# Performance work log

Hardware: AMD Instinct MI355X
Metric: run time of the kernel (lower is better)

The kernel has to match this reference:

```python
import jax, jax.numpy as jnp
import numpy as np

L = 4        # num_layers
D = 64       # in_channels == hidden_channels
OUT = 1      # out_channels
N = 50000    # nodes
E = 800000   # edges
G = 64       # graphs in batch
EPS = 1e-5


def setup_inputs() -> dict:
    key = jax.random.key(0)
    ks = jax.random.split(key, 16)
    s = 1.0 / np.sqrt(D)
    inp = {
        "x": jax.random.normal(ks[0], (N, D), jnp.float32),
        "edge_index": jax.random.randint(ks[1], (2, E), 0, N, jnp.int32),
        "batch": jnp.sort(jax.random.randint(ks[2], (N,), 0, G, jnp.int32)),
        # per-layer GNLayer params (stacked over L)
        "Wm1": jax.random.uniform(ks[3], (L, D, D), jnp.float32, -s, s),
        "bm1": jnp.zeros((L, D), jnp.float32),
        "Wm2": jax.random.uniform(ks[4], (L, D, D), jnp.float32, -s, s),
        "bm2": jnp.zeros((L, D), jnp.float32),
        "Wr": jax.random.uniform(ks[5], (L, D, D), jnp.float32, -s, s),
        "br": jnp.zeros((L, D), jnp.float32),
        "a_conv": jnp.full((L,), 0.25, jnp.float32),     # PReLU slopes
        "gamma": jnp.ones((L, D), jnp.float32),
        "beta": jnp.zeros((L, D), jnp.float32),
        # MLP head
        "Wh1": jax.random.uniform(ks[6], (D, D), jnp.float32, -s, s),
        "bh1": jnp.zeros((D,), jnp.float32),
        "Wh2": jax.random.uniform(ks[7], (D, OUT), jnp.float32, -s, s),
        "bh2": jnp.zeros((OUT,), jnp.float32),
        "a_head": jnp.float32(0.25),
    }
    return inp


def _prelu(v, a):
    return jnp.where(v >= 0, v, a * v)


def reference(x, edge_index, batch, Wm1, bm1, Wm2, bm2, Wr, br, a_conv,
              gamma, beta, Wh1, bh1, Wh2, bh2, a_head):
    src, dst = edge_index[0], edge_index[1]
    h = x
    for i in range(L):
        # GNLayer: message MLP on source features, sum-aggregate at dst, + root transform
        m = jax.nn.relu(h[src] @ Wm1[i] + bm1[i]) @ Wm2[i] + bm2[i]   # [E, D]
        agg = jax.ops.segment_sum(m, dst, num_segments=N)              # [N, D]
        h = agg + h @ Wr[i] + br[i]
        # PReLU
        h = _prelu(h, a_conv[i])
        # BatchNorm over the node dimension (training-mode batch stats)
        mu = jnp.mean(h, axis=0)
        var = jnp.var(h, axis=0)
        h = gamma[i] * (h - mu) * jax.lax.rsqrt(var + EPS) + beta[i]
    # global_mean_pool over graphs
    sums = jax.ops.segment_sum(h, batch, num_segments=G)               # [G, D]
    cnts = jax.ops.segment_sum(jnp.ones((N, 1), h.dtype), batch, num_segments=G)
    g = sums / jnp.maximum(cnts, 1.0)
    # MLP head
    out = _prelu(g @ Wh1 + bh1, a_head) @ Wh2 + bh2                    # [G, OUT]
    return out
```

## Files before the change

kernel.cpp:

```cpp
#include <hip/hip_runtime.h>
#include <hip/hip_fp16.h>

#define D 64


__global__ __launch_bounds__(256) void hist_kernel(const int* __restrict__ dst,
                                                   int* __restrict__ cnt, int E) {
  int e = blockIdx.x * 256 + threadIdx.x;
  if (e < E) atomicAdd(&cnt[dst[e]], 1);
}

__global__ __launch_bounds__(1024) void scan_partial_kernel(const int* __restrict__ cnt,
                                                            int* __restrict__ bsum, int N) {
  __shared__ int lds[1024];
  int i = blockIdx.x * 1024 + threadIdx.x;
  lds[threadIdx.x] = (i < N) ? cnt[i] : 0;
  __syncthreads();
  for (int off = 512; off > 0; off >>= 1) {
    if (threadIdx.x < off) lds[threadIdx.x] += lds[threadIdx.x + off];
    __syncthreads();
  }
  if (threadIdx.x == 0) bsum[blockIdx.x] = lds[0];
}

__global__ void scan_bsum_kernel(int* __restrict__ bsum, int nb,
                                 int* __restrict__ row_ptr, int N, int E) {
  int tid = threadIdx.x;
  int o = (tid < nb) ? bsum[tid] : 0;
  int v = o;
  for (int off = 1; off < 64; off <<= 1) {
    int t = __shfl_up(v, off, 64);
    if (tid >= off) v += t;
  }
  if (tid < nb) bsum[tid] = v - o;
  if (tid == 0) row_ptr[N] = E;
}

__global__ __launch_bounds__(1024) void scan_final_kernel(const int* __restrict__ cnt,
                                                          const int* __restrict__ bsum,
                                                          int* __restrict__ row_ptr,
                                                          int* __restrict__ cursor, int N) {
  __shared__ int lds[1024];
  int tid = threadIdx.x;
  int i = blockIdx.x * 1024 + tid;
  int v = (i < N) ? cnt[i] : 0;
  lds[tid] = v;
  __syncthreads();
  for (int off = 1; off < 1024; off <<= 1) {
    int t = (tid >= off) ? lds[tid - off] : 0;
    __syncthreads();
    lds[tid] += t;
    __syncthreads();
  }
  if (i < N) {
    int excl = bsum[blockIdx.x] + lds[tid] - v;
    row_ptr[i] = excl;
    cursor[i] = excl;
  }
}

__global__ __launch_bounds__(256) void scatter_kernel(const int* __restrict__ srcs,
                                                      const int* __restrict__ dst,
                                                      int* __restrict__ cursor,
                                                      int* __restrict__ csr_src, int E) {
  int e = blockIdx.x * 256 + threadIdx.x;
  if (e < E) {
    int p = atomicAdd(&cursor[dst[e]], 1);
    csr_src[p] = srcs[e];
  }
}


__global__ __launch_bounds__(256, 4) void node_mlp_kernel(
    const float* __restrict__ hin, const float* __restrict__ bnS, const float* __restrict__ bnSS,
    const float* __restrict__ gammaL, const float* __restrict__ betaL,
    const float* __restrict__ W1, const float* __restrict__ b1,
    const float* __restrict__ W2, const float* __restrict__ b2,
    __half* __restrict__ Rout, float* __restrict__ HRout, int N) {
  __shared__ float2 w12[D * D];
  __shared__ float hrow[32][D];
  const int tid = threadIdx.x;
  for (int i = tid; i < D * D; i += 256) w12[i] = make_float2(W1[i], W2[i]);
  const int c = tid & 63;
  const int w = tid >> 6;
  float sc = 1.f, sh = 0.f;
  if (bnS) {
    float invN = 1.f / (float)N;
    float mu = bnS[c] * invN;
    float var = bnSS[c] * invN - mu * mu;
    float s = gammaL[c] * rsqrtf(var + 1e-5f);
    sc = s;
    sh = betaL[c] - mu * s;
  }
  const float bb1 = b1[c], bb2 = b2[c];
  const int ntiles = (N + 31) >> 5;
  for (int t = blockIdx.x; t < ntiles; t += gridDim.x) {
    const int base = t * 32;
    __syncthreads();
#pragma unroll
    for (int j = 0; j < 8; ++j) {
      int r = 4 * j + w;
      int row = base + r;
      float v = (row < N) ? hin[(size_t)row * D + c] : 0.f;
      hrow[r][c] = v * sc + sh;
    }
    __syncthreads();
    float a1[8], a2[8];
#pragma unroll
    for (int j = 0; j < 8; ++j) { a1[j] = bb1; a2[j] = bb2; }
    for (int k = 0; k < D; k += 4) {
      const float2 wa = w12[(k + 0) * D + c];
      const float2 wb = w12[(k + 1) * D + c];
      const float2 wc = w12[(k + 2) * D + c];
      const float2 wd = w12[(k + 3) * D + c];
#pragma unroll
      for (int j = 0; j < 8; ++j) {
        const float4 h4 = *(const float4*)&hrow[w * 8 + j][k];
        a1[j] += h4.x * wa.x + h4.y * wb.x + h4.z * wc.x + h4.w * wd.x;
        a2[j] += h4.x * wa.y + h4.y * wb.y + h4.z * wc.y + h4.w * wd.y;
      }
    }
#pragma unroll
    for (int j = 0; j < 8; ++j) {
      int row = base + w * 8 + j;
      if (row < N) {
        Rout[(size_t)row * D + c] = __float2half(fmaxf(a1[j], 0.f));
        HRout[(size_t)row * D + c] = a2[j];
      }
    }
  }
}


__device__ __forceinline__ float lane_bcast(float v, int lane) {
  return __int_as_float(__builtin_amdgcn_readlane(__float_as_int(v), lane));
}
__device__ __forceinline__ int lane_bcast_i(int v, int lane) {
  return __builtin_amdgcn_readlane(v, lane);
}

__global__ __launch_bounds__(256) void agg_kernel(const int* __restrict__ row_ptr,
                                                  const int* __restrict__ csr_src,
                                                  const __half* __restrict__ Rm,
                                                  const float* __restrict__ HRm,
                                                  const float* __restrict__ W2m,
                                                  const float* __restrict__ b2m,
                                                  const float* __restrict__ aconv,
                                                  float* __restrict__ hout,
                                                  float* __restrict__ bnsum,
                                                  float* __restrict__ bnsumsq, int N) {
  __shared__ float w2[D * D];
  __shared__ float red[4][D];
  __shared__ float red2[4][D];
  const int tid = threadIdx.x;
  const int c = tid & 63;
  const int w = tid >> 6;
  const int q = c & 15;
  const int eg = c >> 4;
  for (int i = tid; i < D * D; i += 256) w2[i] = W2m[i];
  const float alpha = *aconv;
  const float bb = b2m[c];
  const int NW = gridDim.x * 4;
  float psum = 0.f, psumsq = 0.f;
  __syncthreads();

  int n = blockIdx.x * 4 + w;
  int e0 = 0, e1 = 0, idx = 0;
  if (n < N) {
    e0 = row_ptr[n];
    e1 = row_ptr[n + 1];
    int m = e1 - e0;
    if (m > 64) m = 64;
    if (m > 0) idx = csr_src[e0 + (c < m ? c : m - 1)];
  }
  while (n < N) {
    const int n2 = n + NW;
    int e0n = 0, e1n = 0, idxn = 0;
    if (n2 < N) {
      e0n = row_ptr[n2];
      e1n = row_ptr[n2 + 1];
      int mn = e1n - e0n;
      if (mn > 64) mn = 64;
      if (mn > 0) idxn = csr_src[e0n + (c < mn ? c : mn - 1)];
    }
    const int deg = e1 - e0;
    float acc0 = 0.f, acc1 = 0.f, acc2 = 0.f, acc3 = 0.f;
    int kb = 0;
    int curidx = idx;
    while (kb < deg) {
      int m = deg - kb;
      if (m > 64) m = 64;
      if (kb > 0) curidx = csr_src[e0 + kb + (c < m ? c : m - 1)];
      int j = 0;
      for (; j + 3 < m; j += 4) {
        const int s = __shfl(curidx, j + eg, 64);
        const uint2 rv = *(const uint2*)(Rm + (size_t)s * D + (q << 2));
        const float2 f01 = __half22float2(*(const __half2*)&rv.x);
        const float2 f23 = __half22float2(*(const __half2*)&rv.y);
        acc0 += f01.x;
        acc1 += f01.y;
        acc2 += f23.x;
        acc3 += f23.y;
      }
      for (; j < m; ++j) {
        const int s = lane_bcast_i(curidx, j);
        if (eg == 0) {
          const uint2 rv = *(const uint2*)(Rm + (size_t)s * D + (q << 2));
          const float2 f01 = __half22float2(*(const __half2*)&rv.x);
          const float2 f23 = __half22float2(*(const __half2*)&rv.y);
          acc0 += f01.x;
          acc1 += f01.y;
          acc2 += f23.x;
          acc3 += f23.y;
        }
      }
      kb += m;
    }
    acc0 += __shfl_xor(acc0, 16, 64);
    acc1 += __shfl_xor(acc1, 16, 64);
    acc2 += __shfl_xor(acc2, 16, 64);
    acc3 += __shfl_xor(acc3, 16, 64);
    acc0 += __shfl_xor(acc0, 32, 64);
    acc1 += __shfl_xor(acc1, 32, 64);
    acc2 += __shfl_xor(acc2, 32, 64);
    acc3 += __shfl_xor(acc3, 32, 64);
    const float degf = (float)deg;
    float o0 = bb * degf + HRm[(size_t)n * D + c];
    float o1 = 0.f, o2 = 0.f, o3 = 0.f;
#pragma unroll
    for (int kk = 0; kk < D; kk += 4) {
      const int src = kk >> 2;
      o0 += lane_bcast(acc0, src) * w2[(kk + 0) * D + c];
      o1 += lane_bcast(acc1, src) * w2[(kk + 1) * D + c];
      o2 += lane_bcast(acc2, src) * w2[(kk + 2) * D + c];
      o3 += lane_bcast(acc3, src) * w2[(kk + 3) * D + c];
    }
    const float o = (o0 + o1) + (o2 + o3);
    const float h2 = (o >= 0.f) ? o : alpha * o;
    hout[(size_t)n * D + c] = h2;
    psum += h2;
    psumsq += h2 * h2;
    n = n2;
    e0 = e0n;
    e1 = e1n;
    idx = idxn;
  }
  red[w][c] = psum;
  red2[w][c] = psumsq;
  __syncthreads();
  if (w == 0) {
    float s = red[0][c] + red[1][c] + red[2][c] + red[3][c];
    float ss = red2[0][c] + red2[1][c] + red2[2][c] + red2[3][c];
    atomicAdd(&bnsum[c], s);
    atomicAdd(&bnsumsq[c], ss);
  }
}


__global__ __launch_bounds__(256) void pool_head_kernel(
    const float* __restrict__ h, const float* __restrict__ bnS, const float* __restrict__ bnSS,
    const float* __restrict__ gammaL, const float* __restrict__ betaL,
    const int* __restrict__ batch, const float* __restrict__ Wh1, const float* __restrict__ bh1,
    const float* __restrict__ Wh2, const float* __restrict__ bh2,
    const float* __restrict__ ahead, float* __restrict__ out, int N) {
  const int g = blockIdx.x;
  const int tid = threadIdx.x;
  const int c = tid & 63;
  const int w = tid >> 6;
  float sc, sh;
  {
    float invN = 1.f / (float)N;
    float mu = bnS[c] * invN;
    float var = bnSS[c] * invN - mu * mu;
    float s = gammaL[c] * rsqrtf(var + 1e-5f);
    sc = s;
    sh = betaL[c] - mu * s;
  }
  int s0, s1;
  {
    int lo = 0, hi = N;
    while (lo < hi) { int mid = (lo + hi) >> 1; if (batch[mid] < g) lo = mid + 1; else hi = mid; }
    s0 = lo;
    lo = s0; hi = N;
    while (lo < hi) { int mid = (lo + hi) >> 1; if (batch[mid] < g + 1) lo = mid + 1; else hi = mid; }
    s1 = lo;
  }
  float sum = 0.f;
  for (int r = s0 + w; r < s1; r += 4) sum += h[(size_t)r * D + c] * sc + sh;
  __shared__ float red[4][D];
  __shared__ float mean[D];
  red[w][c] = sum;
  __syncthreads();
  if (tid < D) {
    float cnt = (float)(s1 - s0);
    mean[c] = (red[0][c] + red[1][c] + red[2][c] + red[3][c]) / fmaxf(cnt, 1.0f);
  }
  __syncthreads();
  if (tid < D) {
    int j = tid;
    float a = bh1[j];
#pragma unroll
    for (int k = 0; k < D; ++k) a += mean[k] * Wh1[k * D + j];
    float al = *ahead;
    float v = (a >= 0.f) ? a : al * a;
    float pval = v * Wh2[j];
    for (int off = 32; off > 0; off >>= 1) pval += __shfl_down(pval, off, 64);
    if (j == 0) out[g] = pval + bh2[0];
  }
}


extern "C" void kernel_launch(void* const* d_in, const int* in_sizes, int n_in,
                              void* d_out, int out_size, void* d_ws, size_t ws_size,
                              hipStream_t stream) {
  const float* x = (const float*)d_in[0];
  const int* ei = (const int*)d_in[1];
  const int* batch = (const int*)d_in[2];
  const float* Wm1 = (const float*)d_in[3];
  const float* bm1 = (const float*)d_in[4];
  const float* Wm2 = (const float*)d_in[5];
  const float* bm2 = (const float*)d_in[6];
  const float* Wr = (const float*)d_in[7];
  const float* br = (const float*)d_in[8];
  const float* aconv = (const float*)d_in[9];
  const float* gamma = (const float*)d_in[10];
  const float* beta = (const float*)d_in[11];
  const float* Wh1 = (const float*)d_in[12];
  const float* bh1 = (const float*)d_in[13];
  const float* Wh2 = (const float*)d_in[14];
  const float* bh2 = (const float*)d_in[15];
  const float* ahead = (const float*)d_in[16];

  const int N = in_sizes[0] / D;
  const int E = in_sizes[1] / 2;
  const int L = in_sizes[3] / (D * D);
  const int G = out_size;

  const int* srcs = ei;
  const int* dsts = ei + E;

  char* p = (char*)d_ws;
  auto alloc = [&](size_t bytes) {
    char* r = p;
    p += (bytes + 255) & ~(size_t)255;
    return r;
  };
  int* row_ptr = (int*)alloc((size_t)(N + 1) * 4);
  int* cursor = (int*)alloc((size_t)N * 4);
  int* bsum = (int*)alloc(64 * 4);
  int* csr_src = (int*)alloc((size_t)E * 4);
  __half* Rbuf = (__half*)alloc((size_t)N * D * 2);
  float* HRbuf = (float*)alloc((size_t)N * D * 4);
  float* hbuf = (float*)alloc((size_t)N * D * 4);
  float* bnsum = (float*)alloc((size_t)L * D * 4 * 2);
  float* bnsumsq = bnsum + (size_t)L * D;

  hipMemsetAsync(row_ptr, 0, (size_t)((char*)(cursor + N) - (char*)row_ptr), stream);
  hipMemsetAsync(bnsum, 0, (size_t)L * D * 4 * 2, stream);

  const int nb = (N + 1023) / 1024;
  hist_kernel<<<(E + 255) / 256, 256, 0, stream>>>(dsts, cursor, E);
  scan_partial_kernel<<<nb, 1024, 0, stream>>>(cursor, bsum, N);
  scan_bsum_kernel<<<1, 64, 0, stream>>>(bsum, nb, row_ptr, N, E);
  scan_final_kernel<<<nb, 1024, 0, stream>>>(cursor, bsum, row_ptr, cursor, N);
  scatter_kernel<<<(E + 255) / 256, 256, 0, stream>>>(srcs, dsts, cursor, csr_src, E);

  const int ntiles = (N + 31) / 32;

  const float* hin = x;
  const float* bnS = nullptr;
  const float* bnSS = nullptr;
  const float* gmL = nullptr;
  const float* btL = nullptr;
  for (int l = 0; l < L; ++l) {
    node_mlp_kernel<<<ntiles, 256, 0, stream>>>(hin, bnS, bnSS, gmL, btL,
                                                Wm1 + (size_t)l * D * D, bm1 + l * D,
                                                Wr + (size_t)l * D * D, br + l * D,
                                                Rbuf, HRbuf, N);
    agg_kernel<<<2048, 256, 0, stream>>>(row_ptr, csr_src, Rbuf, HRbuf,
                                         Wm2 + (size_t)l * D * D, bm2 + l * D, aconv + l,
                                         hbuf, bnsum + l * D, bnsumsq + l * D, N);
    hin = hbuf;
    bnS = bnsum + l * D;
    bnSS = bnsumsq + l * D;
    gmL = gamma + l * D;
    btL = beta + l * D;
  }

  pool_head_kernel<<<G, 256, 0, stream>>>(hbuf, bnS, bnSS, gmL, btL, batch,
                                          Wh1, bh1, Wh2, bh2, ahead, (float*)d_out, N);
}
```

Before: 590.8 us.

## Fuse whole GNN pipeline into one persistent cooperative kernel with grid syncs

Replaces the separate launches (histogram, scan, scatter, per-layer MLP and aggregation, pool/head) with one cooperative persistent kernel that separates phases with grid-wide syncs. Launch gaps and the memsets go away. The layer-0 MLP now overlaps the CSR build, and pooling uses chunked atomics into a per-graph sum buffer instead of a G-block sequential scan. In exchange the grid is limited to resident blocks, each grid.sync has a cost, the shared-memory union may lower occupancy, and the scan assumes at most 256 partial blocks.

```diff
diff --git a/kernel.cpp b/kernel.cpp
--- a/kernel.cpp
+++ b/kernel.cpp
@@ -1,98 +1,65 @@
 #include <hip/hip_runtime.h>
 #include <hip/hip_fp16.h>
+#include <hip/hip_cooperative_groups.h>
 
 #define D 64
 
-
-__global__ __launch_bounds__(256) void hist_kernel(const int* __restrict__ dst,
-                                                   int* __restrict__ cnt, int E) {
-  int e = blockIdx.x * 256 + threadIdx.x;
-  if (e < E) atomicAdd(&cnt[dst[e]], 1);
-}
-
-__global__ __launch_bounds__(1024) void scan_partial_kernel(const int* __restrict__ cnt,
-                                                            int* __restrict__ bsum, int N) {
-  __shared__ int lds[1024];
-  int i = blockIdx.x * 1024 + threadIdx.x;
-  lds[threadIdx.x] = (i < N) ? cnt[i] : 0;
-  __syncthreads();
-  for (int off = 512; off > 0; off >>= 1) {
-    if (threadIdx.x < off) lds[threadIdx.x] += lds[threadIdx.x + off];
-    __syncthreads();
-  }
-  if (threadIdx.x == 0) bsum[blockIdx.x] = lds[0];
-}
-
-__global__ void scan_bsum_kernel(int* __restrict__ bsum, int nb,
-                                 int* __restrict__ row_ptr, int N, int E) {
-  int tid = threadIdx.x;
-  int o = (tid < nb) ? bsum[tid] : 0;
-  int v = o;
-  for (int off = 1; off < 64; off <<= 1) {
-    int t = __shfl_up(v, off, 64);
-    if (tid >= off) v += t;
-  }
-  if (tid < nb) bsum[tid] = v - o;
-  if (tid == 0) row_ptr[N] = E;
-}
-
-__global__ __launch_bounds__(1024) void scan_final_kernel(const int* __restrict__ cnt,
-                                                          const int* __restrict__ bsum,
-                                                          int* __restrict__ row_ptr,
-                                                          int* __restrict__ cursor, int N) {
-  __shared__ int lds[1024];
-  int tid = threadIdx.x;
-  int i = blockIdx.x * 1024 + tid;
-  int v = (i < N) ? cnt[i] : 0;
-  lds[tid] = v;
-  __syncthreads();
-  for (int off = 1; off < 1024; off <<= 1) {
-    int t = (tid >= off) ? lds[tid - off] : 0;
-    __syncthreads();
-    lds[tid] += t;
-    __syncthreads();
-  }
-  if (i < N) {
-    int excl = bsum[blockIdx.x] + lds[tid] - v;
-    row_ptr[i] = excl;
-    cursor[i] = excl;
-  }
-}
-
-__global__ __launch_bounds__(256) void scatter_kernel(const int* __restrict__ srcs,
-                                                      const int* __restrict__ dst,
-                                                      int* __restrict__ cursor,
-                                                      int* __restrict__ csr_src, int E) {
-  int e = blockIdx.x * 256 + threadIdx.x;
-  if (e < E) {
-    int p = atomicAdd(&cursor[dst[e]], 1);
-    csr_src[p] = srcs[e];
-  }
-}
-
-
-__global__ __launch_bounds__(256, 4) void node_mlp_kernel(
-    const float* __restrict__ hin, const float* __restrict__ bnS, const float* __restrict__ bnSS,
-    const float* __restrict__ gammaL, const float* __restrict__ betaL,
-    const float* __restrict__ W1, const float* __restrict__ b1,
-    const float* __restrict__ W2, const float* __restrict__ b2,
-    __half* __restrict__ Rout, float* __restrict__ HRout, int N) {
-  __shared__ float2 w12[D * D];
-  __shared__ float hrow[32][D];
+namespace cg = cooperative_groups;
+
+struct Params {
+  const float* x;
+  const int* srcs;
+  const int* dsts;
+  const int* batch;
+  const float* Wm1; const float* bm1;
+  const float* Wm2; const float* bm2;
+  const float* Wr;  const float* br;
+  const float* aconv;
+  const float* gamma; const float* beta;
+  const float* Wh1; const float* bh1;
+  const float* Wh2; const float* bh2;
+  const float* ahead;
+  int* row_ptr; int* cursor; int* bsum2; int* csr_src;
+  __half* Rbuf; float* HRbuf; float* hbuf;
+  float* bnsum;
+  float* gsum;
+  float* out;
+  int N, E, G, L;
+};
+
+struct SM_MLP { float2 w12[D * D]; float hrow[32][D]; };
+struct SM_AGG { float w2[D * D]; float red[4][D]; float red2[4][D]; };
+struct SM_SCAN { int si[256]; };
+struct SM_HEAD { float mean[D]; };
+union SMU { SM_MLP mlp; SM_AGG agg; SM_SCAN scan; SM_HEAD head; };
+
+__device__ __forceinline__ float lane_bcast(float v, int lane) {
+  return __int_as_float(__builtin_amdgcn_readlane(__float_as_int(v), lane));
+}
+__device__ __forceinline__ int lane_bcast_i(int v, int lane) {
+  return __builtin_amdgcn_readlane(v, lane);
+}
+
+__device__ void mlp_phase(const Params& P, SMU& sm, int l, const float* __restrict__ hin) {
   const int tid = threadIdx.x;
-  for (int i = tid; i < D * D; i += 256) w12[i] = make_float2(W1[i], W2[i]);
+  const float* W1 = P.Wm1 + (size_t)l * D * D;
+  const float* W2 = P.Wr + (size_t)l * D * D;
+  for (int i = tid; i < D * D; i += 256) sm.mlp.w12[i] = make_float2(W1[i], W2[i]);
   const int c = tid & 63;
   const int w = tid >> 6;
   float sc = 1.f, sh = 0.f;
-  if (bnS) {
-    float invN = 1.f / (float)N;
+  if (l > 0) {
+    const float* bnS = P.bnsum + (size_t)(l - 1) * D;
+    const float* bnSS = bnS + (size_t)P.L * D;
+    float invN = 1.f / (float)P.N;
     float mu = bnS[c] * invN;
     float var = bnSS[c] * invN - mu * mu;
-    float s = gammaL[c] * rsqrtf(var + 1e-5f);
+    float s = P.gamma[(size_t)(l - 1) * D + c] * rsqrtf(var + 1e-5f);
     sc = s;
-    sh = betaL[c] - mu * s;
-  }
-  const float bb1 = b1[c], bb2 = b2[c];
+    sh = P.beta[(size_t)(l - 1) * D + c] - mu * s;
+  }
+  const float bb1 = P.bm1[(size_t)l * D + c], bb2 = P.br[(size_t)l * D + c];
+  const int N = P.N;
   const int ntiles = (N + 31) >> 5;
   for (int t = blockIdx.x; t < ntiles; t += gridDim.x) {
     const int base = t * 32;
@@ -102,20 +69,20 @@
       int r = 4 * j + w;
       int row = base + r;
       float v = (row < N) ? hin[(size_t)row * D + c] : 0.f;
-      hrow[r][c] = v * sc + sh;
+      sm.mlp.hrow[r][c] = v * sc + sh;
     }
     __syncthreads();
     float a1[8], a2[8];
 #pragma unroll
     for (int j = 0; j < 8; ++j) { a1[j] = bb1; a2[j] = bb2; }
     for (int k = 0; k < D; k += 4) {
-      const float2 wa = w12[(k + 0) * D + c];
-      const float2 wb = w12[(k + 1) * D + c];
-      const float2 wc = w12[(k + 2) * D + c];
-      const float2 wd = w12[(k + 3) * D + c];
+      const float2 wa = sm.mlp.w12[(k + 0) * D + c];
+      const float2 wb = sm.mlp.w12[(k + 1) * D + c];
+      const float2 wc = sm.mlp.w12[(k + 2) * D + c];
+      const float2 wd = sm.mlp.w12[(k + 3) * D + c];
 #pragma unroll
       for (int j = 0; j < 8; ++j) {
-        const float4 h4 = *(const float4*)&hrow[w * 8 + j][k];
+        const float4 h4 = *(const float4*)&sm.mlp.hrow[w * 8 + j][k];
         a1[j] += h4.x * wa.x + h4.y * wb.x + h4.z * wc.x + h4.w * wd.x;
         a2[j] += h4.x * wa.y + h4.y * wb.y + h4.z * wc.y + h4.w * wd.y;
       }
@@ -124,43 +91,30 @@
     for (int j = 0; j < 8; ++j) {
       int row = base + w * 8 + j;
       if (row < N) {
-        Rout[(size_t)row * D + c] = __float2half(fmaxf(a1[j], 0.f));
-        HRout[(size_t)row * D + c] = a2[j];
+        P.Rbuf[(size_t)row * D + c] = __float2half(fmaxf(a1[j], 0.f));
+        P.HRbuf[(size_t)row * D + c] = a2[j];
       }
     }
   }
 }
 
-
-__device__ __forceinline__ float lane_bcast(float v, int lane) {
-  return __int_as_float(__builtin_amdgcn_readlane(__float_as_int(v), lane));
-}
-__device__ __forceinline__ int lane_bcast_i(int v, int lane) {
-  return __builtin_amdgcn_readlane(v, lane);
-}
-
-__global__ __launch_bounds__(256) void agg_kernel(const int* __restrict__ row_ptr,
-                                                  const int* __restrict__ csr_src,
-                                                  const __half* __restrict__ Rm,
-                                                  const float* __restrict__ HRm,
-                                                  const float* __restrict__ W2m,
-                                                  const float* __restrict__ b2m,
-                                                  const float* __restrict__ aconv,
-                                                  float* __restrict__ hout,
-                                                  float* __restrict__ bnsum,
-                                                  float* __restrict__ bnsumsq, int N) {
-  __shared__ float w2[D * D];
-  __shared__ float red[4][D];
-  __shared__ float red2[4][D];
+__device__ void agg_phase(const Params& P, SMU& sm, int l) {
   const int tid = threadIdx.x;
   const int c = tid & 63;
   const int w = tid >> 6;
   const int q = c & 15;
   const int eg = c >> 4;
-  for (int i = tid; i < D * D; i += 256) w2[i] = W2m[i];
-  const float alpha = *aconv;
-  const float bb = b2m[c];
+  const float* W2m = P.Wm2 + (size_t)l * D * D;
+  for (int i = tid; i < D * D; i += 256) sm.agg.w2[i] = W2m[i];
+  const float alpha = P.aconv[l];
+  const float bb = P.bm2[(size_t)l * D + c];
+  float* bnsum_l = P.bnsum + (size_t)l * D;
+  float* bnsumsq_l = bnsum_l + (size_t)P.L * D;
+  const int N = P.N;
   const int NW = gridDim.x * 4;
+  const int* __restrict__ row_ptr = P.row_ptr;
+  const int* __restrict__ csr_src = P.csr_src;
+  const __half* __restrict__ Rm = P.Rbuf;
   float psum = 0.f, psumsq = 0.f;
   __syncthreads();
 
@@ -225,19 +179,19 @@
     acc2 += __shfl_xor(acc2, 32, 64);
     acc3 += __shfl_xor(acc3, 32, 64);
     const float degf = (float)deg;
-    float o0 = bb * degf + HRm[(size_t)n * D + c];
+    float o0 = bb * degf + P.HRbuf[(size_t)n * D + c];
     float o1 = 0.f, o2 = 0.f, o3 = 0.f;
 #pragma unroll
     for (int kk = 0; kk < D; kk += 4) {
       const int src = kk >> 2;
-      o0 += lane_bcast(acc0, src) * w2[(kk + 0) * D + c];
-      o1 += lane_bcast(acc1, src) * w2[(kk + 1) * D + c];
-      o2 += lane_bcast(acc2, src) * w2[(kk + 2) * D + c];
-      o3 += lane_bcast(acc3, src) * w2[(kk + 3) * D + c];
+      o0 += lane_bcast(acc0, src) * sm.agg.w2[(kk + 0) * D + c];
+      o1 += lane_bcast(acc1, src) * sm.agg.w2[(kk + 1) * D + c];
+      o2 += lane_bcast(acc2, src) * sm.agg.w2[(kk + 2) * D + c];
+      o3 += lane_bcast(acc3, src) * sm.agg.w2[(kk + 3) * D + c];
     }
     const float o = (o0 + o1) + (o2 + o3);
     const float h2 = (o >= 0.f) ? o : alpha * o;
-    hout[(size_t)n * D + c] = h2;
+    P.hbuf[(size_t)n * D + c] = h2;
     psum += h2;
     psumsq += h2 * h2;
     n = n2;
@@ -245,67 +199,152 @@
     e1 = e1n;
     idx = idxn;
   }
-  red[w][c] = psum;
-  red2[w][c] = psumsq;
+  sm.agg.red[w][c] = psum;
+  sm.agg.red2[w][c] = psumsq;
   __syncthreads();
   if (w == 0) {
-    float s = red[0][c] + red[1][c] + red[2][c] + red[3][c];
-    float ss = red2[0][c] + red2[1][c] + red2[2][c] + red2[3][c];
-    atomicAdd(&bnsum[c], s);
-    atomicAdd(&bnsumsq[c], ss);
-  }
-}
-
-
-__global__ __launch_bounds__(256) void pool_head_kernel(
-    const float* __restrict__ h, const float* __restrict__ bnS, const float* __restrict__ bnSS,
-    const float* __restrict__ gammaL, const float* __restrict__ betaL,
-    const int* __restrict__ batch, const float* __restrict__ Wh1, const float* __restrict__ bh1,
-    const float* __restrict__ Wh2, const float* __restrict__ bh2,
-    const float* __restrict__ ahead, float* __restrict__ out, int N) {
-  const int g = blockIdx.x;
+    float s = sm.agg.red[0][c] + sm.agg.red[1][c] + sm.agg.red[2][c] + sm.agg.red[3][c];
+    float ss = sm.agg.red2[0][c] + sm.agg.red2[1][c] + sm.agg.red2[2][c] + sm.agg.red2[3][c];
+    atomicAdd(&bnsum_l[c], s);
+    atomicAdd(&bnsumsq_l[c], ss);
+  }
+}
+
+__global__ __launch_bounds__(256, 4) void fused_gnn_kernel(Params P) {
+  __shared__ SMU sm;
+  cg::grid_group grid = cg::this_grid();
   const int tid = threadIdx.x;
-  const int c = tid & 63;
-  const int w = tid >> 6;
-  float sc, sh;
+  const int gtid = blockIdx.x * 256 + tid;
+  const int gsz = gridDim.x * 256;
+  const int N = P.N, E = P.E, G = P.G, L = P.L;
+
+  for (int i = gtid; i < N; i += gsz) P.cursor[i] = 0;
+  for (int i = gtid; i < 2 * L * D; i += gsz) P.bnsum[i] = 0.f;
+  for (int i = gtid; i < G * D; i += gsz) P.gsum[i] = 0.f;
+  mlp_phase(P, sm, 0, P.x);
+  grid.sync();
+
+  for (int e = gtid; e < E; e += gsz) atomicAdd(&P.cursor[P.dsts[e]], 1);
+  grid.sync();
+
+  const int nsb = (N + 255) >> 8;
+  if (blockIdx.x < nsb) {
+    int i = blockIdx.x * 256 + tid;
+    int v = (i < N) ? P.cursor[i] : 0;
+    sm.scan.si[tid] = v;
+    __syncthreads();
+    for (int off = 128; off > 0; off >>= 1) {
+      if (tid < off) sm.scan.si[tid] += sm.scan.si[tid + off];
+      __syncthreads();
+    }
+    if (tid == 0) P.bsum2[blockIdx.x] = sm.scan.si[0];
+  }
+  grid.sync();
+
+  if (blockIdx.x == 0) {
+    int v = (tid < nsb) ? P.bsum2[tid] : 0;
+    sm.scan.si[tid] = v;
+    __syncthreads();
+    for (int off = 1; off < 256; off <<= 1) {
+      int t2 = (tid >= off) ? sm.scan.si[tid - off] : 0;
+      __syncthreads();
+      sm.scan.si[tid] += t2;
+      __syncthreads();
+    }
+    if (tid < nsb) P.bsum2[tid] = sm.scan.si[tid] - v;
+  }
+  grid.sync();
+
+  if (blockIdx.x < nsb) {
+    int i = blockIdx.x * 256 + tid;
+    int v = (i < N) ? P.cursor[i] : 0;
+    sm.scan.si[tid] = v;
+    __syncthreads();
+    for (int off = 1; off < 256; off <<= 1) {
+      int t2 = (tid >= off) ? sm.scan.si[tid - off] : 0;
+      __syncthreads();
+      sm.scan.si[tid] += t2;
+      __syncthreads();
+    }
+    if (i < N) {
+      int excl = P.bsum2[blockIdx.x] + sm.scan.si[tid] - v;
+      P.row_ptr[i] = excl;
+      P.cursor[i] = excl;
+    }
+  }
+  if (gtid == 0) P.row_ptr[N] = E;
+  grid.sync();
+
+  for (int e = gtid; e < E; e += gsz) {
+    int pp = atomicAdd(&P.cursor[P.dsts[e]], 1);
+    P.csr_src[pp] = P.srcs[e];
+  }
+  grid.sync();
+
+  agg_phase(P, sm, 0);
+  grid.sync();
+  for (int l = 1; l < L; ++l) {
+    mlp_phase(P, sm, l, P.hbuf);
+    grid.sync();
+    agg_phase(P, sm, l);
+    grid.sync();
+  }
+
   {
-    float invN = 1.f / (float)N;
-    float mu = bnS[c] * invN;
-    float var = bnSS[c] * invN - mu * mu;
-    float s = gammaL[c] * rsqrtf(var + 1e-5f);
-    sc = s;
-    sh = betaL[c] - mu * s;
-  }
-  int s0, s1;
-  {
-    int lo = 0, hi = N;
-    while (lo < hi) { int mid = (lo + hi) >> 1; if (batch[mid] < g) lo = mid + 1; else hi = mid; }
-    s0 = lo;
-    lo = s0; hi = N;
-    while (lo < hi) { int mid = (lo + hi) >> 1; if (batch[mid] < g + 1) lo = mid + 1; else hi = mid; }
-    s1 = lo;
-  }
-  float sum = 0.f;
-  for (int r = s0 + w; r < s1; r += 4) sum += h[(size_t)r * D + c] * sc + sh;
-  __shared__ float red[4][D];
-  __shared__ float mean[D];
-  red[w][c] = sum;
-  __syncthreads();
-  if (tid < D) {
-    float cnt = (float)(s1 - s0);
-    mean[c] = (red[0][c] + red[1][c] + red[2][c] + red[3][c]) / fmaxf(cnt, 1.0f);
-  }
-  __syncthreads();
-  if (tid < D) {
-    int j = tid;
-    float a = bh1[j];
-#pragma unroll
-    for (int k = 0; k < D; ++k) a += mean[k] * Wh1[k * D + j];
-    float al = *ahead;
-    float v = (a >= 0.f) ? a : al * a;
-    float pval = v * Wh2[j];
-    for (int off = 32; off > 0; off >>= 1) pval += __shfl_down(pval, off, 64);
-    if (j == 0) out[g] = pval + bh2[0];
+    const int c = tid & 63;
+    const int w = tid >> 6;
+    const int nchunks = (N + 63) >> 6;
+    for (int ch = blockIdx.x; ch < nchunks; ch += gridDim.x) {
+      const int r0 = ch * 64;
+      const int rend = (r0 + 64 < N) ? r0 + 64 : N;
+      int curg = -1;
+      float acc = 0.f;
+      for (int r = r0 + w; r < rend; r += 4) {
+        int g = P.batch[r];
+        float v = P.hbuf[(size_t)r * D + c];
+        if (g != curg) {
+          if (curg >= 0) atomicAdd(&P.gsum[(size_t)curg * D + c], acc);
+          acc = 0.f;
+          curg = g;
+        }
+        acc += v;
+      }
+      if (curg >= 0) atomicAdd(&P.gsum[(size_t)curg * D + c], acc);
+    }
+  }
+  grid.sync();
+
+  if (blockIdx.x < G) {
+    const int g = blockIdx.x;
+    if (tid < D) {
+      const int c = tid;
+      const float* bnS = P.bnsum + (size_t)(L - 1) * D;
+      const float* bnSS = bnS + (size_t)L * D;
+      float invN = 1.f / (float)N;
+      float mu = bnS[c] * invN;
+      float var = bnSS[c] * invN - mu * mu;
+      float s = P.gamma[(size_t)(L - 1) * D + c] * rsqrtf(var + 1e-5f);
+      float sh = P.beta[(size_t)(L - 1) * D + c] - mu * s;
+      int lo = 0, hi = N;
+      while (lo < hi) { int mid = (lo + hi) >> 1; if (P.batch[mid] < g) lo = mid + 1; else hi = mid; }
+      int s0 = lo;
+      lo = s0; hi = N;
+      while (lo < hi) { int mid = (lo + hi) >> 1; if (P.batch[mid] < g + 1) lo = mid + 1; else hi = mid; }
+      float cnt = fmaxf((float)(lo - s0), 1.0f);
+      sm.head.mean[c] = (P.gsum[(size_t)g * D + c] / cnt) * s + sh;
+    }
+    __syncthreads();
+    if (tid < D) {
+      int j = tid;
+      float a = P.bh1[j];
+#pragma unroll
+      for (int k = 0; k < D; ++k) a += sm.head.mean[k] * P.Wh1[k * D + j];
+      float al = *P.ahead;
+      float v = (a >= 0.f) ? a : al * a;
+      float pval = v * P.Wh2[j];
+      for (int off = 32; off > 0; off >>= 1) pval += __shfl_down(pval, off, 64);
+      if (j == 0) P.out[g] = pval + P.bh2[0];
+    }
   }
 }
 
@@ -316,28 +355,11 @@
   const float* x = (const float*)d_in[0];
   const int* ei = (const int*)d_in[1];
   const int* batch = (const int*)d_in[2];
-  const float* Wm1 = (const float*)d_in[3];
-  const float* bm1 = (const float*)d_in[4];
-  const float* Wm2 = (const float*)d_in[5];
-  const float* bm2 = (const float*)d_in[6];
-  const float* Wr = (const float*)d_in[7];
-  const float* br = (const float*)d_in[8];
-  const float* aconv = (const float*)d_in[9];
-  const float* gamma = (const float*)d_in[10];
-  const float* beta = (const float*)d_in[11];
-  const float* Wh1 = (const float*)d_in[12];
-  const float* bh1 = (const float*)d_in[13];
-  const float* Wh2 = (const float*)d_in[14];
-  const float* bh2 = (const float*)d_in[15];
-  const float* ahead = (const float*)d_in[16];
 
   const int N = in_sizes[0] / D;
   const int E = in_sizes[1] / 2;
   const int L = in_sizes[3] / (D * D);
   const int G = out_size;
-
-  const int* srcs = ei;
-  const int* dsts = ei + E;
 
   char* p = (char*)d_ws;
   auto alloc = [&](size_t bytes) {
@@ -347,46 +369,59 @@
   };
   int* row_ptr = (int*)alloc((size_t)(N + 1) * 4);
   int* cursor = (int*)alloc((size_t)N * 4);
-  int* bsum = (int*)alloc(64 * 4);
+  int* bsum2 = (int*)alloc(256 * 4);
   int* csr_src = (int*)alloc((size_t)E * 4);
   __half* Rbuf = (__half*)alloc((size_t)N * D * 2);
   float* HRbuf = (float*)alloc((size_t)N * D * 4);
   float* hbuf = (float*)alloc((size_t)N * D * 4);
   float* bnsum = (float*)alloc((size_t)L * D * 4 * 2);
-  float* bnsumsq = bnsum + (size_t)L * D;
-
-  hipMemsetAsync(row_ptr, 0, (size_t)((char*)(cursor + N) - (char*)row_ptr), stream);
-  hipMemsetAsync(bnsum, 0, (size_t)L * D * 4 * 2, stream);
-
-  const int nb = (N + 1023) / 1024;
-  hist_kernel<<<(E + 255) / 256, 256, 0, stream>>>(dsts, cursor, E);
-  scan_partial_kernel<<<nb, 1024, 0, stream>>>(cursor, bsum, N);
-  scan_bsum_kernel<<<1, 64, 0, stream>>>(bsum, nb, row_ptr, N, E);
-  scan_final_kernel<<<nb, 1024, 0, stream>>>(cursor, bsum, row_ptr, cursor, N);
-  scatter_kernel<<<(E + 255) / 256, 256, 0, stream>>>(srcs, dsts, cursor, csr_src, E);
-
-  const int ntiles = (N + 31) / 32;
-
-  const float* hin = x;
-  const float* bnS = nullptr;
-  const float* bnSS = nullptr;
-  const float* gmL = nullptr;
-  const float* btL = nullptr;
-  for (int l = 0; l < L; ++l) {
-    node_mlp_kernel<<<ntiles, 256, 0, stream>>>(hin, bnS, bnSS, gmL, btL,
-                                                Wm1 + (size_t)l * D * D, bm1 + l * D,
-                                                Wr + (size_t)l * D * D, br + l * D,
-                                                Rbuf, HRbuf, N);
-    agg_kernel<<<2048, 256, 0, stream>>>(row_ptr, csr_src, Rbuf, HRbuf,
-                                         Wm2 + (size_t)l * D * D, bm2 + l * D, aconv + l,
-                                         hbuf, bnsum + l * D, bnsumsq + l * D, N);
-    hin = hbuf;
-    bnS = bnsum + l * D;
-    bnSS = bnsumsq + l * D;
-    gmL = gamma + l * D;
-    btL = beta + l * D;
-  }
-
-  pool_head_kernel<<<G, 256, 0, stream>>>(hbuf, bnS, bnSS, gmL, btL, batch,
-                                          Wh1, bh1, Wh2, bh2, ahead, (float*)d_out, N);
-}
+  float* gsum = (float*)alloc((size_t)G * D * 4);
+
+  Params P;
+  P.x = x;
+  P.srcs = ei;
+  P.dsts = ei + E;
+  P.batch = batch;
+  P.Wm1 = (const float*)d_in[3];
+  P.bm1 = (const float*)d_in[4];
+  P.Wm2 = (const float*)d_in[5];
+  P.bm2 = (const float*)d_in[6];
+  P.Wr = (const float*)d_in[7];
+  P.br = (const float*)d_in[8];
+  P.aconv = (const float*)d_in[9];
+  P.gamma = (const float*)d_in[10];
+  P.beta = (const float*)d_in[11];
+  P.Wh1 = (const float*)d_in[12];
+  P.bh1 = (const float*)d_in[13];
+  P.Wh2 = (const float*)d_in[14];
+  P.bh2 = (const float*)d_in[15];
+  P.ahead = (const float*)d_in[16];
+  P.row_ptr = row_ptr;
+  P.cursor = cursor;
+  P.bsum2 = bsum2;
+  P.csr_src = csr_src;
+  P.Rbuf = Rbuf;
+  P.HRbuf = HRbuf;
+  P.hbuf = hbuf;
+  P.bnsum = bnsum;
+  P.gsum = gsum;
+  P.out = (float*)d_out;
+  P.N = N;
+  P.E = E;
+  P.G = G;
+  P.L = L;
+
+  int dev = 0;
+  hipGetDevice(&dev);
+  int numCU = 256;
+  hipDeviceGetAttribute(&numCU, hipDeviceAttributeMultiprocessorCount, dev);
+  int maxbpc = 0;
+  if (hipOccupancyMaxActiveBlocksPerMultiprocessor(&maxbpc, fused_gnn_kernel, 256, 0) !=
+          hipSuccess ||
+      maxbpc < 1)
+    maxbpc = 3;
+  int blocks = numCU * maxbpc;
+
+  void* args[] = {&P};
+  hipLaunchCooperativeKernel((void*)fused_gnn_kernel, dim3(blocks), dim3(256), args, 0, stream);
+}
```

Result: slower. 1.428 ms (+141.7%).
